# Kernel optimization log

Measured on AMD Instinct MI355X. Metric: run time of the kernel, lower is better.

The kernel has to match this reference:

```python
import jax, jax.numpy as jnp
import numpy as np

INFTY_APPROX = 1e+30
ROTARY_BASE = 10000.0
D_HEAD = 128


def rope(x):
    # x: [B, H, T, D]
    *_, length, width = x.shape
    half = width // 2
    positions = jnp.arange(length)[:, None].astype(x.dtype)          # [T, 1]
    dims = jnp.arange(half).astype(x.dtype)                           # [half]
    ang_freqs = jnp.power(ROTARY_BASE, -dims / half)[None, :]         # [1, half]
    radians = positions * ang_freqs                                   # [T, half]
    cos = jnp.cos(radians)[None, None].astype(x.dtype)                # [1,1,T,half]
    sin = jnp.sin(radians)[None, None].astype(x.dtype)
    even, odd = jnp.split(x, 2, axis=-1)
    r_even = even * cos - odd * sin
    r_odd = even * sin + odd * cos
    return jnp.concatenate([r_even, r_odd], axis=-1)


def setup_inputs() -> dict:
    key = jax.random.key(0)
    ks = jax.random.split(key, 5)
    B, T, M, D = 4, 2048, 1024, D_HEAD
    H = M // D
    x = jax.random.normal(ks[0], (B, T, M), dtype=jnp.float32)
    scale = M ** -0.5
    wq = jax.random.normal(ks[1], (H, M, D), dtype=jnp.float32) * scale
    wk = jax.random.normal(ks[2], (H, M, D), dtype=jnp.float32) * scale
    wv = jax.random.normal(ks[3], (H, M, D), dtype=jnp.float32) * scale
    wo = jax.random.normal(ks[4], (H, D, M), dtype=jnp.float32) * scale
    return {"x": x, "wq": wq, "wk": wk, "wv": wv, "wo": wo}


def reference(x, wq, wk, wv, wo):
    # x: [B, T, M]; w{q,k,v}: [H, M, D]; wo: [H, D, M]
    q = jnp.einsum('bim,hmd->bhid', x, wq)
    k = jnp.einsum('bim,hmd->bhid', x, wk)
    v = jnp.einsum('bim,hmd->bhid', x, wv)
    q = rope(q)
    k = rope(k)
    # NOTE: module scales BOTH q and k by d_head**-0.5 (mup-style 1/d overall)
    mult = jnp.asarray(D_HEAD ** -0.5, dtype=x.dtype)
    s = jnp.einsum('bhid,bhjd->bhij', q * mult, k * mult)
    T = s.shape[-1]
    i = jnp.arange(T)[:, None]
    j = jnp.arange(T)[None, :]
    mask = (i < j).astype(s.dtype)[None, None]  # future positions masked
    s = s - jnp.asarray(INFTY_APPROX, dtype=s.dtype) * mask
    p = jax.nn.softmax(s, axis=-1)
    o = jnp.einsum('bhij,bhjd->bhid', p, v)
    r = jnp.einsum('bhid,hdm->bim', o, wo)
    return r
```

## Files before the change

kernel.cpp:

```cpp
#include <hip/hip_runtime.h>
#include <math.h>


typedef unsigned short u16;
typedef __attribute__((ext_vector_type(8))) short short8;
typedef __attribute__((ext_vector_type(4))) float floatx4;

#define MFMA_B16(a, b, c) __builtin_amdgcn_mfma_f32_16x16x32_bf16((a), (b), (c), 0, 0, 0)

__device__ __forceinline__ void async_cp16(const void* g, void* l) {
  __builtin_amdgcn_global_load_lds(
      (const __attribute__((address_space(1))) unsigned int*)g,
      (__attribute__((address_space(3))) unsigned int*)l, 16, 0, 0);
}

__device__ __forceinline__ u16 f2bf(float f) {
  unsigned u = __float_as_uint(f);
  u += 0x7FFFu + ((u >> 16) & 1u);
  return (u16)(u >> 16);
}

__device__ __forceinline__ unsigned cvt_pk_bf16(float lo, float hi) {
  unsigned r;
  asm("v_cvt_pk_bf16_f32 %0, %1, %2" : "=v"(r) : "v"(lo), "v"(hi));
  return r;
}

__device__ __forceinline__ int swz8(int row, int chunk) { return ((chunk ^ (row & 7)) << 3); }


__global__ void conv_x(const float* __restrict__ xf, u16* __restrict__ xb) {
  int idx = (blockIdx.x * 256 + threadIdx.x) * 4;
  float4 v = *(const float4*)(xf + idx);
  ushort4 o = make_ushort4(f2bf(v.x), f2bf(v.y), f2bf(v.z), f2bf(v.w));
  *(ushort4*)(xb + idx) = o;
}

__global__ void prep_wqkv(const float* __restrict__ wq, const float* __restrict__ wk,
                          const float* __restrict__ wv, u16* __restrict__ wT) {
  __shared__ float tile[32][33];
  const float* src = (blockIdx.z == 0) ? wq : (blockIdx.z == 1) ? wk : wv;
  u16* dst = wT + (size_t)blockIdx.z * 1024 * 1024;
  int h = blockIdx.y >> 2, dt = blockIdx.y & 3;
  int m0 = blockIdx.x * 32, d0 = dt * 32;
  int tx = threadIdx.x, ty = threadIdx.y;
#pragma unroll
  for (int i = 0; i < 4; i++) {
    int r = ty + i * 8;
    tile[r][tx] = src[((size_t)h * 1024 + m0 + r) * 128 + d0 + tx];
  }
  __syncthreads();
#pragma unroll
  for (int i = 0; i < 4; i++) {
    int r = ty + i * 8;
    dst[((size_t)h * 128 + d0 + r) * 1024 + m0 + tx] = f2bf(tile[tx][r]);
  }
}

__global__ void prep_wo(const float* __restrict__ wo, u16* __restrict__ woT) {
  __shared__ float tile[32][33];
  int r0 = blockIdx.y * 32, c0 = blockIdx.x * 32;
  int tx = threadIdx.x, ty = threadIdx.y;
#pragma unroll
  for (int i = 0; i < 4; i++) {
    int r = ty + i * 8;
    tile[r][tx] = wo[(size_t)(r0 + r) * 1024 + c0 + tx];
  }
  __syncthreads();
#pragma unroll
  for (int i = 0; i < 4; i++) {
    int r = ty + i * 8;
    woT[(size_t)(c0 + r) * 1024 + r0 + tx] = f2bf(tile[tx][r]);
  }
}

__global__ void prep_rope(float2* __restrict__ tab) {
  int idx = blockIdx.x * 256 + threadIdx.x;
  int t = idx >> 6, d = idx & 63;
  const float c1 = -0.20762050593046015f;
  float freq = exp2f((float)d * c1);
  float rad = (float)t * freq;
  float s, c;
  sincosf(rad, &s, &c);
  tab[idx] = make_float2(c, s);
}

template <int MODE>
__launch_bounds__(256, 2)
__global__ void gemm_bt(const u16* __restrict__ A, const u16* __restrict__ Bt,
                        void* __restrict__ out0, u16* __restrict__ out_k,
                        u16* __restrict__ out_v, const float2* __restrict__ ropetab) {
  __shared__ u16 smem[16384];
  u16* As = smem;
  u16* Bs = smem + 8192;
  const int tid = threadIdx.x;
  const int w = tid >> 6, lane = tid & 63, quad = lane >> 4, l15 = lane & 15;
  const int row0 = blockIdx.x * 128;
  const int by = blockIdx.y;
  const int n0 = by * 128;

  floatx4 acc[2][8] = {};

  for (int kt = 0; kt < 16; ++kt) {
    __syncthreads();
#pragma unroll
    for (int i = 0; i < 4; i++) {
      int cidx = (w * 4 + i) * 64 + lane;
      int r = cidx >> 3, c = cidx & 7, cg = c ^ (r & 7);
      async_cp16(A + (size_t)(row0 + r) * 1024 + kt * 64 + cg * 8, As + (w * 4 + i) * 512);
      async_cp16(Bt + (size_t)(n0 + r) * 1024 + kt * 64 + cg * 8, Bs + (w * 4 + i) * 512);
    }
    __syncthreads();
#pragma unroll
    for (int ks = 0; ks < 2; ks++) {
      short8 af[2];
#pragma unroll
      for (int mi = 0; mi < 2; mi++) {
        int r = w * 32 + mi * 16 + l15;
        af[mi] = *(const short8*)(As + r * 64 + swz8(r, ks * 4 + quad));
      }
#pragma unroll
      for (int ni = 0; ni < 8; ni++) {
        int n = ni * 16 + l15;
        short8 bf = *(const short8*)(Bs + n * 64 + swz8(n, ks * 4 + quad));
        acc[0][ni] = MFMA_B16(af[0], bf, acc[0][ni]);
        acc[1][ni] = MFMA_B16(af[1], bf, acc[1][ni]);
      }
    }
  }
  __syncthreads();

  if (MODE == 0) {
    int sel = by >> 3, h = by & 7;
    if (sel < 2) {
      u16* dst = sel ? out_k : (u16*)out0;
#pragma unroll
      for (int mi = 0; mi < 2; mi++) {
#pragma unroll
        for (int reg = 0; reg < 4; reg++) {
          int row = row0 + w * 32 + mi * 16 + quad * 4 + reg;
          int b = row >> 11, t = row & 2047;
          u16* drow = dst + ((size_t)(b * 8 + h) * 2048 + t) * 128;
#pragma unroll
          for (int ni = 0; ni < 4; ni++) {
            int d = ni * 16 + l15;
            float2 cs = ropetab[t * 64 + d];
            float e = acc[mi][ni][reg], o = acc[mi][ni + 4][reg];
            drow[d] = f2bf(e * cs.x - o * cs.y);
            drow[d + 64] = f2bf(e * cs.y + o * cs.x);
          }
        }
      }
    } else {
#pragma unroll
      for (int mi = 0; mi < 2; mi++) {
#pragma unroll
        for (int reg = 0; reg < 4; reg++) {
          int r = w * 32 + mi * 16 + quad * 4 + reg;
#pragma unroll
          for (int ni = 0; ni < 8; ni++) {
            int col = ni * 16 + l15;
            smem[r * 128 + swz8(r, col >> 3) + (col & 7)] = f2bf(acc[mi][ni][reg]);
          }
        }
      }
      __syncthreads();
      int tl = tid & 127, dg = tid >> 7;
      int row = row0 + tl;
      int b = row >> 11, t = row & 2047;
      u16* vdst = out_v + (size_t)(b * 8 + h) * 128 * 2048;
#pragma unroll
      for (int dd = 0; dd < 64; dd++) {
        int d = dg * 64 + dd;
        u16 val = smem[tl * 128 + swz8(tl, d >> 3) + (d & 7)];
        vdst[(size_t)d * 2048 + t] = val;
      }
    }
  } else {
    float* outf = (float*)out0;
#pragma unroll
    for (int mi = 0; mi < 2; mi++) {
#pragma unroll
      for (int reg = 0; reg < 4; reg++) {
        int row = row0 + w * 32 + mi * 16 + quad * 4 + reg;
#pragma unroll
        for (int ni = 0; ni < 8; ni++) {
          outf[(size_t)row * 1024 + n0 + ni * 16 + l15] = acc[mi][ni][reg];
        }
      }
    }
  }
}

__device__ __forceinline__ void stage_kv(const u16* kb, const u16* vb, int jt,
                                         u16* Kd, u16* Vd, int w, int lane) {
#pragma unroll
  for (int i = 0; i < 4; i++) {
    int cidx = (w * 4 + i) * 64 + lane;
    int rK = cidx >> 4, cK = cidx & 15, gK = cK ^ (rK & 7);
    async_cp16(kb + (size_t)(jt * 64 + rK) * 128 + gK * 8, Kd + (w * 4 + i) * 512);
    int rV = cidx >> 3, cV = cidx & 7, gV = cV ^ (rV & 7);
    async_cp16(vb + (size_t)rV * 2048 + jt * 64 + gV * 8, Vd + (w * 4 + i) * 512);
  }
}

__launch_bounds__(256, 2)
__global__ void flash_attn(const u16* __restrict__ Q, const u16* __restrict__ Kw,
                           const u16* __restrict__ Vw, u16* __restrict__ O) {
  __shared__ u16 smem[40960];
  u16* const Ps = smem + 32768;

  const int tid = threadIdx.x;
  const int w = tid >> 6, lane = tid & 63, quad = lane >> 4, l15 = lane & 15;

  const int id = (int)blockIdx.x;
  const int bh = id & 31;
  const int p = (id >> 5) & 7;
  const int qt = (id >> 8) ? (15 - p) : p;

  const u16* qb = Q + (size_t)bh * 2048 * 128;
  const u16* kb = Kw + (size_t)bh * 2048 * 128;
  const u16* vb = Vw + (size_t)bh * 128 * 2048;
  const int b = bh >> 3, h = bh & 7;
  const float SC = 0.011271055f;

  const int iw = qt * 128 + w * 32;
  const int nj = 2 * qt + 2;

  short8 qf[2][4];
#pragma unroll
  for (int mi = 0; mi < 2; mi++) {
    int qrow = iw + mi * 16 + l15;
#pragma unroll
    for (int ks = 0; ks < 4; ks++)
      qf[mi][ks] = *(const short8*)(qb + (size_t)qrow * 128 + ks * 32 + quad * 8);
  }

  floatx4 accO[2][8] = {};
  float lsum[2] = {0.f, 0.f};

  stage_kv(kb, vb, 0, smem, smem + 16384, w, lane);

  int cur = 0;
  for (int jt = 0; jt < nj; ++jt) {
    __syncthreads();

    if (jt + 1 < nj)
      stage_kv(kb, vb, jt + 1, smem + (cur ^ 1) * 8192, smem + 16384 + (cur ^ 1) * 8192, w, lane);

    const u16* Ks = smem + cur * 8192;
    const u16* Vs = smem + 16384 + cur * 8192;
    const int j0 = jt * 64;

    if (j0 <= iw + 31) {
      const bool partial = (j0 + 63 > iw);

      floatx4 sa[4][2] = {};
      __builtin_amdgcn_s_setprio(1);
#pragma unroll
      for (int jj = 0; jj < 4; jj++) {
        const bool ok1 = (j0 + jj * 16 <= iw + 31);
        if (!ok1) continue;
        const bool ok0 = (j0 + jj * 16 <= iw + 15);
#pragma unroll
        for (int ks = 0; ks < 4; ks++) {
          int j = jj * 16 + l15;
          short8 kf = *(const short8*)(Ks + j * 128 + swz8(j, ks * 4 + quad));
          if (ok0) sa[jj][0] = MFMA_B16(kf, qf[0][ks], sa[jj][0]);
          sa[jj][1] = MFMA_B16(kf, qf[1][ks], sa[jj][1]);
        }
      }
      __builtin_amdgcn_s_setprio(0);

#pragma unroll
      for (int mi = 0; mi < 2; mi++) {
        const int prow = w * 32 + mi * 16 + l15;
        const int ig = iw + mi * 16 + l15;
#pragma unroll
        for (int jj = 0; jj < 4; jj++) {
          float pv[4];
#pragma unroll
          for (int r = 0; r < 4; r++) {
            float s = sa[jj][mi][r] * SC;
            if (partial) {
              int jg = j0 + jj * 16 + quad * 4 + r;
              if (jg > ig) s = -1e30f;
            }
            pv[r] = exp2f(s);
            lsum[mi] += pv[r];
          }
          uint2 pk;
          pk.x = cvt_pk_bf16(pv[0], pv[1]);
          pk.y = cvt_pk_bf16(pv[2], pv[3]);
          int jc = jj * 16 + quad * 4;
          *(uint2*)(Ps + prow * 64 + swz8(prow, jc >> 3) + (jc & 7)) = pk;
        }
      }

      __builtin_amdgcn_s_setprio(1);
#pragma unroll
      for (int k2 = 0; k2 < 2; k2++) {
        short8 pa[2];
#pragma unroll
        for (int mi = 0; mi < 2; mi++) {
          int prow = w * 32 + mi * 16 + l15;
          pa[mi] = *(const short8*)(Ps + prow * 64 + swz8(prow, k2 * 4 + quad));
        }
#pragma unroll
        for (int nt = 0; nt < 8; nt++) {
          int dr = nt * 16 + l15;
          short8 vf = *(const short8*)(Vs + dr * 64 + swz8(dr, k2 * 4 + quad));
          accO[0][nt] = MFMA_B16(pa[0], vf, accO[0][nt]);
          accO[1][nt] = MFMA_B16(pa[1], vf, accO[1][nt]);
        }
      }
      __builtin_amdgcn_s_setprio(0);
    }
    cur ^= 1;
  }

#pragma unroll
  for (int mi = 0; mi < 2; mi++) {
    lsum[mi] += __shfl_xor(lsum[mi], 16);
    lsum[mi] += __shfl_xor(lsum[mi], 32);
  }

#pragma unroll
  for (int mi = 0; mi < 2; mi++) {
#pragma unroll
    for (int r = 0; r < 4; r++) {
      float lr = __shfl(lsum[mi], quad * 4 + r);
      float inv = 1.0f / fmaxf(lr, 1e-30f);
      int t = iw + mi * 16 + quad * 4 + r;
#pragma unroll
      for (int nt = 0; nt < 8; nt++) {
        O[(((size_t)b * 2048 + t) * 8 + h) * 128 + nt * 16 + l15] =
            f2bf(accO[mi][nt][r] * inv);
      }
    }
  }
}

extern "C" void kernel_launch(void* const* d_in, const int* in_sizes, int n_in,
                              void* d_out, int out_size, void* d_ws, size_t ws_size,
                              hipStream_t stream) {
  const float* x = (const float*)d_in[0];
  const float* wq = (const float*)d_in[1];
  const float* wk = (const float*)d_in[2];
  const float* wv = (const float*)d_in[3];
  const float* wo = (const float*)d_in[4];
  float* out = (float*)d_out;

  char* ws = (char*)d_ws;
  const size_t SZ = 16777216;
  u16* x_bf = (u16*)(ws);
  u16* q_ws = (u16*)(ws + SZ);
  u16* k_ws = (u16*)(ws + 2 * SZ);
  u16* v_ws = (u16*)(ws + 3 * SZ);
  u16* o_ws = (u16*)(ws + 4 * SZ);
  u16* wT = (u16*)(ws + 5 * SZ);
  u16* woT = (u16*)(ws + 5 * SZ + 6291456);
  float2* tab = (float2*)(ws + 5 * SZ + 6291456 + 2097152);

  conv_x<<<8192, 256, 0, stream>>>(x, x_bf);
  prep_wqkv<<<dim3(32, 32, 3), dim3(32, 8), 0, stream>>>(wq, wk, wv, wT);
  prep_wo<<<dim3(32, 32), dim3(32, 8), 0, stream>>>(wo, woT);
  prep_rope<<<512, 256, 0, stream>>>(tab);
  gemm_bt<0><<<dim3(64, 24), 256, 0, stream>>>(x_bf, wT, q_ws, k_ws, v_ws, tab);
  flash_attn<<<512, 256, 0, stream>>>(q_ws, k_ws, v_ws, o_ws);
  gemm_bt<1><<<dim3(64, 8), 256, 0, stream>>>(o_ws, woT, out, nullptr, nullptr, nullptr);
}
```

Baseline: 256.5 us.

## Keep softmax probabilities in registers by permuting V layout, fold scale into RoPE

The V tensor's sequence index is stored with a permutation so the S-accumulator fragment of the QK^T MFMA can be fed directly as the A operand of the PV MFMA. This removes the LDS round-trip for P and shrinks flash-attention shared memory. The softmax scale is folded into the RoPE cos/sin table so the per-element multiply disappears. A fully masked second k-chunk is also skipped. The cost is a strided, scattered V store pattern and a dependence on the exact permutation matching the MFMA lane mapping.

```diff
diff --git a/kernel.cpp b/kernel.cpp
--- a/kernel.cpp
+++ b/kernel.cpp
@@ -78,11 +78,12 @@
   int idx = blockIdx.x * 256 + threadIdx.x;
   int t = idx >> 6, d = idx & 63;
   const float c1 = -0.20762050593046015f;
+  const float SQ = 0.10616522f;
   float freq = exp2f((float)d * c1);
   float rad = (float)t * freq;
   float s, c;
   sincosf(rad, &s, &c);
-  tab[idx] = make_float2(c, s);
+  tab[idx] = make_float2(c * SQ, s * SQ);
 }
 
 template <int MODE>
@@ -168,12 +169,13 @@
       int tl = tid & 127, dg = tid >> 7;
       int row = row0 + tl;
       int b = row >> 11, t = row & 2047;
+      int tp = (t & ~31) | ((((t >> 2) & 3) << 3) | (t & 3) | ((t & 16) >> 2));
       u16* vdst = out_v + (size_t)(b * 8 + h) * 128 * 2048;
 #pragma unroll
       for (int dd = 0; dd < 64; dd++) {
         int d = dg * 64 + dd;
         u16 val = smem[tl * 128 + swz8(tl, d >> 3) + (d & 7)];
-        vdst[(size_t)d * 2048 + t] = val;
+        vdst[(size_t)d * 2048 + tp] = val;
       }
     }
   } else {
@@ -207,8 +209,7 @@
 __launch_bounds__(256, 2)
 __global__ void flash_attn(const u16* __restrict__ Q, const u16* __restrict__ Kw,
                            const u16* __restrict__ Vw, u16* __restrict__ O) {
-  __shared__ u16 smem[40960];
-  u16* const Ps = smem + 32768;
+  __shared__ u16 smem[32768];
 
   const int tid = threadIdx.x;
   const int w = tid >> 6, lane = tid & 63, quad = lane >> 4, l15 = lane & 15;
@@ -222,7 +223,6 @@
   const u16* kb = Kw + (size_t)bh * 2048 * 128;
   const u16* vb = Vw + (size_t)bh * 128 * 2048;
   const int b = bh >> 3, h = bh & 7;
-  const float SC = 0.011271055f;
 
   const int iw = qt * 128 + w * 32;
   const int nj = 2 * qt + 2;
@@ -272,16 +272,16 @@
       }
       __builtin_amdgcn_s_setprio(0);
 
+      unsigned pk_[2][2][4];
 #pragma unroll
       for (int mi = 0; mi < 2; mi++) {
-        const int prow = w * 32 + mi * 16 + l15;
         const int ig = iw + mi * 16 + l15;
 #pragma unroll
         for (int jj = 0; jj < 4; jj++) {
           float pv[4];
 #pragma unroll
           for (int r = 0; r < 4; r++) {
-            float s = sa[jj][mi][r] * SC;
+            float s = sa[jj][mi][r];
             if (partial) {
               int jg = j0 + jj * 16 + quad * 4 + r;
               if (jg > ig) s = -1e30f;
@@ -289,29 +289,30 @@
             pv[r] = exp2f(s);
             lsum[mi] += pv[r];
           }
-          uint2 pk;
-          pk.x = cvt_pk_bf16(pv[0], pv[1]);
-          pk.y = cvt_pk_bf16(pv[2], pv[3]);
-          int jc = jj * 16 + quad * 4;
-          *(uint2*)(Ps + prow * 64 + swz8(prow, jc >> 3) + (jc & 7)) = pk;
+          pk_[mi][jj >> 1][(jj & 1) * 2 + 0] = cvt_pk_bf16(pv[0], pv[1]);
+          pk_[mi][jj >> 1][(jj & 1) * 2 + 1] = cvt_pk_bf16(pv[2], pv[3]);
         }
       }
 
       __builtin_amdgcn_s_setprio(1);
 #pragma unroll
       for (int k2 = 0; k2 < 2; k2++) {
-        short8 pa[2];
+        if (k2 == 1 && j0 + 32 > iw + 31) continue;
+        union {
+          unsigned u[4];
+          short8 s8;
+        } pa[2];
 #pragma unroll
         for (int mi = 0; mi < 2; mi++) {
-          int prow = w * 32 + mi * 16 + l15;
-          pa[mi] = *(const short8*)(Ps + prow * 64 + swz8(prow, k2 * 4 + quad));
+#pragma unroll
+          for (int dw = 0; dw < 4; dw++) pa[mi].u[dw] = pk_[mi][k2][dw];
         }
 #pragma unroll
         for (int nt = 0; nt < 8; nt++) {
           int dr = nt * 16 + l15;
           short8 vf = *(const short8*)(Vs + dr * 64 + swz8(dr, k2 * 4 + quad));
-          accO[0][nt] = MFMA_B16(pa[0], vf, accO[0][nt]);
-          accO[1][nt] = MFMA_B16(pa[1], vf, accO[1][nt]);
+          accO[0][nt] = MFMA_B16(pa[0].s8, vf, accO[0][nt]);
+          accO[1][nt] = MFMA_B16(pa[1].s8, vf, accO[1][nt]);
         }
       }
       __builtin_amdgcn_s_setprio(0);
```

Result: no change. 251.6 us (-1.9%).
